# Kernel optimization log

Hardware: AMD Instinct MI355X
Metric: run time of the kernel (lower is better)

## Reference

```python
import jax, jax.numpy as jnp
import numpy as np

LN_EPS = 1e-5

def setup_inputs() -> dict:
    key = jax.random.key(0)
    ks = jax.random.split(key, 10)
    L, B, D, C, O = 512, 2, 256, 128, 64
    s_in = 1.0 / np.sqrt(D)
    s_ch = 1.0 / np.sqrt(C)
    return {
        "x": jax.random.normal(ks[0], (L, B, D), dtype=jnp.float32),
        "ln_gamma": jnp.ones((D,), dtype=jnp.float32),
        "ln_beta": jnp.zeros((D,), dtype=jnp.float32),
        "w1": jax.random.uniform(ks[1], (D, C), jnp.float32, -s_in, s_in),
        "b1": jax.random.uniform(ks[2], (C,), jnp.float32, -s_in, s_in),
        "w2": jax.random.uniform(ks[3], (D, C), jnp.float32, -s_in, s_in),
        "b2": jax.random.uniform(ks[4], (C,), jnp.float32, -s_in, s_in),
        "w3": jax.random.uniform(ks[5], (C, O), jnp.float32, -s_ch, s_ch),
        "b3": jax.random.uniform(ks[6], (O,), jnp.float32, -s_ch, s_ch),
        "w4": jax.random.uniform(ks[7], (C, O), jnp.float32, -s_ch, s_ch),
    }

def _layernorm(x, gamma, beta):
    mu = jnp.mean(x, axis=-1, keepdims=True)
    var = jnp.mean(jnp.square(x - mu), axis=-1, keepdims=True)
    return (x - mu) * jax.lax.rsqrt(var + LN_EPS) * gamma + beta

def reference(x, ln_gamma, ln_beta, w1, b1, w2, b2, w3, b3, w4):
    # x: (L, B, D) -> (B, L, D)
    xb = jnp.transpose(x, (1, 0, 2))
    xb = _layernorm(xb, ln_gamma, ln_beta)
    a = xb @ w1 + b1  # (B, L, C)
    b = xb @ w2 + b2  # (B, L, C)
    # (a_l * b_m) @ w3  -> contract channel dim directly into output channels
    mul_term = jnp.einsum('blc,bmc,co->blmo', a, b, w3) + b3
    # (a_l - b_m) @ w4  -> distribute linearity to avoid (B,L,L,C) materialization
    a4 = a @ w4  # (B, L, O)
    b4 = b @ w4  # (B, L, O)
    sub_term = a4[:, :, None, :] - b4[:, None, :, :]
    return mul_term + sub_term  # (B, L, L, O)
```

## Files before the change

### kernel.cpp

```cpp
#include <hip/hip_runtime.h>
#include <hip/hip_bf16.h>

#define LL 512
#define BB 2
#define DD 256
#define CC 128
#define OO 64

typedef __attribute__((ext_vector_type(8))) short bf16x8;
typedef __attribute__((ext_vector_type(4))) float f32x4;

__device__ __forceinline__ short f2bf(float v) {
    __hip_bfloat16 h = __float2bfloat16(v);
    return *reinterpret_cast<short*>(&h);
}
__device__ __forceinline__ float bf2f(short s) {
    __hip_bfloat16 h;
    *reinterpret_cast<short*>(&h) = s;
    return __bfloat162float(h);
}

__device__ __forceinline__ float wave_reduce_sum(float v) {
#pragma unroll
    for (int off = 32; off > 0; off >>= 1)
        v += __shfl_down(v, off, 64);
    return v;
}

__global__ __launch_bounds__(256) void prep_kernel(
    const float* __restrict__ x,
    const float* __restrict__ gamma,
    const float* __restrict__ beta,
    const float* __restrict__ w1, const float* __restrict__ b1,
    const float* __restrict__ w2, const float* __restrict__ b2,
    const float* __restrict__ w4, const float* __restrict__ b3,
    const float* __restrict__ w3,
    float* __restrict__ a_ws, short* __restrict__ bact,
    float* __restrict__ a4b3_ws, float* __restrict__ b4_ws,
    short* __restrict__ w3s)
{
    const int blk = blockIdx.x;
    const int t = threadIdx.x;

    if (blk >= BB * LL) {
        const int e  = (blk - BB * LL) * 256 + t;
        const int j  = e & 7;
        const int ln = (e >> 3) & 15;
        const int q  = (e >> 7) & 3;
        const int ks = (e >> 9) & 3;
        const int ot = e >> 11;
        const int c = ks * 32 + q * 8 + j;
        const int o = ot * 16 + ln;
        w3s[e] = f2bf(w3[c * OO + o]);
        return;
    }

    const int b = blk >> 9;
    const int l = blk & (LL - 1);

    __shared__ float ylds[DD];
    __shared__ float ab[2 * CC];
    __shared__ float red[8];

    float xv = x[(l * BB + b) * DD + t];
    float s = wave_reduce_sum(xv);
    if ((t & 63) == 0) red[t >> 6] = s;
    __syncthreads();
    float mu = (red[0] + red[1] + red[2] + red[3]) * (1.0f / DD);
    float xc = xv - mu;
    float s2 = wave_reduce_sum(xc * xc);
    if ((t & 63) == 0) red[4 + (t >> 6)] = s2;
    __syncthreads();
    float var = (red[4] + red[5] + red[6] + red[7]) * (1.0f / DD);
    float y = xc * rsqrtf(var + 1e-5f) * gamma[t] + beta[t];
    ylds[t] = y;
    __syncthreads();

    {
        const int c = t & (CC - 1);
        const float* w = (t < CC) ? w1 : w2;
        const float4* y4 = (const float4*)ylds;
        float acc0 = (t < CC) ? b1[c] : b2[c];
        float acc1 = 0.f, acc2 = 0.f, acc3 = 0.f;
#pragma unroll
        for (int i = 0; i < 64; i += 4) {
            float4 ya = y4[i], yb = y4[i + 1], yc = y4[i + 2], yd = y4[i + 3];
            const float* wp = w + i * 4 * CC + c;
            acc0 = fmaf(ya.x, wp[0 * CC], acc0);
            acc0 = fmaf(ya.y, wp[1 * CC], acc0);
            acc0 = fmaf(ya.z, wp[2 * CC], acc0);
            acc0 = fmaf(ya.w, wp[3 * CC], acc0);
            acc1 = fmaf(yb.x, wp[4 * CC], acc1);
            acc1 = fmaf(yb.y, wp[5 * CC], acc1);
            acc1 = fmaf(yb.z, wp[6 * CC], acc1);
            acc1 = fmaf(yb.w, wp[7 * CC], acc1);
            acc2 = fmaf(yc.x, wp[8 * CC], acc2);
            acc2 = fmaf(yc.y, wp[9 * CC], acc2);
            acc2 = fmaf(yc.z, wp[10 * CC], acc2);
            acc2 = fmaf(yc.w, wp[11 * CC], acc2);
            acc3 = fmaf(yd.x, wp[12 * CC], acc3);
            acc3 = fmaf(yd.y, wp[13 * CC], acc3);
            acc3 = fmaf(yd.z, wp[14 * CC], acc3);
            acc3 = fmaf(yd.w, wp[15 * CC], acc3);
        }
        float accv = (acc0 + acc1) + (acc2 + acc3);
        ab[t] = accv;
        if (t < CC) a_ws[(b * LL + l) * CC + c] = accv;
        else        bact[(b * LL + l) * CC + c] = f2bf(accv);
    }
    __syncthreads();

    if (t < 2 * OO) {
        const int o = t & (OO - 1);
        const float4* s4 = (const float4*)((t < OO) ? ab : (ab + CC));
        float acc0 = (t < OO) ? b3[o] : 0.0f;
        float acc1 = 0.f, acc2 = 0.f, acc3 = 0.f;
#pragma unroll
        for (int i = 0; i < 32; i += 4) {
            float4 sa = s4[i], sb = s4[i + 1], sc = s4[i + 2], sd = s4[i + 3];
            const float* wp = w4 + i * 4 * OO + o;
            acc0 = fmaf(sa.x, wp[0 * OO], acc0);
            acc0 = fmaf(sa.y, wp[1 * OO], acc0);
            acc0 = fmaf(sa.z, wp[2 * OO], acc0);
            acc0 = fmaf(sa.w, wp[3 * OO], acc0);
            acc1 = fmaf(sb.x, wp[4 * OO], acc1);
            acc1 = fmaf(sb.y, wp[5 * OO], acc1);
            acc1 = fmaf(sb.z, wp[6 * OO], acc1);
            acc1 = fmaf(sb.w, wp[7 * OO], acc1);
            acc2 = fmaf(sc.x, wp[8 * OO], acc2);
            acc2 = fmaf(sc.y, wp[9 * OO], acc2);
            acc2 = fmaf(sc.z, wp[10 * OO], acc2);
            acc2 = fmaf(sc.w, wp[11 * OO], acc2);
            acc3 = fmaf(sd.x, wp[12 * OO], acc3);
            acc3 = fmaf(sd.y, wp[13 * OO], acc3);
            acc3 = fmaf(sd.z, wp[14 * OO], acc3);
            acc3 = fmaf(sd.w, wp[15 * OO], acc3);
        }
        float accv = (acc0 + acc1) + (acc2 + acc3);
        ((t < OO) ? a4b3_ws : b4_ws)[(b * LL + l) * OO + o] = accv;
    }
}

__global__ __launch_bounds__(256, 3) void main_kernel(
    const float* __restrict__ a_ws, const short* __restrict__ bact,
    const float* __restrict__ a4b3_ws, const float* __restrict__ b4_ws,
    const short* __restrict__ w3s,
    float* __restrict__ out)
{
    const int bid = blockIdx.x;
    const int mh = bid & 1;
    const int l  = (bid >> 1) & (LL - 1);
    const int b  = bid >> 10;
    const int t  = threadIdx.x;
    const int wave = t >> 6;
    const int lane = t & 63;
    const int ln = lane & 15;
    const int q  = lane >> 4;
    const int mbase = mh * 256 + wave * 64;

    const float* arow = a_ws + (b * LL + l) * CC;
    const short* abase = bact + (size_t)(b * LL + mbase + ln) * CC + q * 8;

    f32x4 acc[4][4];
#pragma unroll
    for (int ot = 0; ot < 4; ++ot)
#pragma unroll
        for (int mt = 0; mt < 4; ++mt)
            acc[ot][mt] = (f32x4){0.f, 0.f, 0.f, 0.f};

#pragma unroll
    for (int ks = 0; ks < 4; ++ks) {
        const float* ap = arow + ks * 32 + q * 8;
        float av[8];
        *(float4*)&av[0] = *(const float4*)ap;
        *(float4*)&av[4] = *(const float4*)(ap + 4);

        bf16x8 wp[4];
#pragma unroll
        for (int ot = 0; ot < 4; ++ot) {
            bf16x8 wr = *(const bf16x8*)(w3s + (((ot * 4 + ks) * 4 + q) << 7) + ln * 8);
            bf16x8 r;
#pragma unroll
            for (int j = 0; j < 8; ++j)
                r[j] = f2bf(bf2f(wr[j]) * av[j]);
            wp[ot] = r;
        }

        bf16x8 bfr[4];
#pragma unroll
        for (int mt = 0; mt < 4; ++mt)
            bfr[mt] = *(const bf16x8*)(abase + mt * 16 * CC + ks * 32);

#pragma unroll
        for (int ot = 0; ot < 4; ++ot)
#pragma unroll
            for (int mt = 0; mt < 4; ++mt)
                acc[ot][mt] = __builtin_amdgcn_mfma_f32_16x16x32_bf16(
                    wp[ot], bfr[mt], acc[ot][mt], 0, 0, 0);
    }

    const float* a4p = a4b3_ws + (b * LL + l) * OO;
    float4 a4v[4];
#pragma unroll
    for (int ot = 0; ot < 4; ++ot)
        a4v[ot] = *(const float4*)(a4p + ot * 16 + q * 4);

#pragma unroll
    for (int mt = 0; mt < 4; ++mt) {
        const int m = mbase + mt * 16 + ln;
        const float* b4p = b4_ws + (size_t)(b * LL + m) * OO;
        float* op = out + ((size_t)(b * LL + l) * LL + m) * OO;
#pragma unroll
        for (int ot = 0; ot < 4; ++ot) {
            float4 bq = *(const float4*)(b4p + ot * 16 + q * 4);
            f32x4 a = acc[ot][mt];
            float4 r;
            r.x = a[0] + a4v[ot].x - bq.x;
            r.y = a[1] + a4v[ot].y - bq.y;
            r.z = a[2] + a4v[ot].z - bq.z;
            r.w = a[3] + a4v[ot].w - bq.w;
            *(float4*)(op + ot * 16 + q * 4) = r;
        }
    }
}

extern "C" void kernel_launch(void* const* d_in, const int* in_sizes, int n_in,
                              void* d_out, int out_size, void* d_ws, size_t ws_size,
                              hipStream_t stream) {
    const float* x     = (const float*)d_in[0];
    const float* gamma = (const float*)d_in[1];
    const float* beta  = (const float*)d_in[2];
    const float* w1    = (const float*)d_in[3];
    const float* b1    = (const float*)d_in[4];
    const float* w2    = (const float*)d_in[5];
    const float* b2    = (const float*)d_in[6];
    const float* w3    = (const float*)d_in[7];
    const float* b3    = (const float*)d_in[8];
    const float* w4    = (const float*)d_in[9];
    float* out = (float*)d_out;

    char* ws = (char*)d_ws;
    float* a_ws    = (float*)ws;
    short* bact    = (short*)(ws + 512 * 1024);
    float* a4b3_ws = (float*)(ws + 768 * 1024);
    float* b4_ws   = (float*)(ws + 1024 * 1024);
    short* w3s     = (short*)(ws + 1280 * 1024);

    prep_kernel<<<BB * LL + 32, 256, 0, stream>>>(x, gamma, beta, w1, b1, w2, b2,
                                                  w4, b3, w3,
                                                  a_ws, bact, a4b3_ws, b4_ws, w3s);
    main_kernel<<<BB * LL * 2, 256, 0, stream>>>(a_ws, bact, a4b3_ws, b4_ws,
                                                 w3s, out);
}
```

Baseline: 194.2 us.

## Precompute per-row scaled W3 fragments in a separate kernel before main GEMM

Adds a wall_kernel that precomputes, for every (b,l) row, W3 scaled elementwise by a[b,l,:] in bf16 and stores it in an extra 16 MB workspace buffer. The main kernel then loads these fragments directly instead of recomputing the bf16 scale-and-convert per MFMA operand. The goal is to cut VALU conversion work and register pressure in the hot loop, and the launch bound rises from 3 to 4 blocks per SIMD. In exchange it adds a kernel launch and about 16 MB of extra global write and read traffic.

```diff
diff --git a/kernel.cpp b/kernel.cpp
--- a/kernel.cpp
+++ b/kernel.cpp
@@ -141,10 +141,38 @@
     }
 }
 
-__global__ __launch_bounds__(256, 3) void main_kernel(
-    const float* __restrict__ a_ws, const short* __restrict__ bact,
+__global__ __launch_bounds__(256) void wall_kernel(
+    const float* __restrict__ a_ws, const short* __restrict__ w3s,
+    short* __restrict__ wall)
+{
+    const int blk = blockIdx.x;
+    const int t = threadIdx.x;
+    const int f0 = t * 4;
+    const int q  = (f0 >> 4) & 3;
+    const int ks = (f0 >> 6) & 3;
+    const int c  = ks * 32 + q * 8;
+
+    const float* ap = a_ws + blk * CC + c;
+    float av[8];
+    *(float4*)&av[0] = *(const float4*)ap;
+    *(float4*)&av[4] = *(const float4*)(ap + 4);
+
+    const short* src = w3s + f0 * 8;
+    short* dst = wall + (size_t)blk * (CC * OO) + f0 * 8;
+#pragma unroll
+    for (int i = 0; i < 4; ++i) {
+        bf16x8 wr = *(const bf16x8*)(src + i * 8);
+        bf16x8 r;
+#pragma unroll
+        for (int j = 0; j < 8; ++j)
+            r[j] = f2bf(bf2f(wr[j]) * av[j]);
+        *(bf16x8*)(dst + i * 8) = r;
+    }
+}
+
+__global__ __launch_bounds__(256, 4) void main_kernel(
+    const short* __restrict__ wall, const short* __restrict__ bact,
     const float* __restrict__ a4b3_ws, const float* __restrict__ b4_ws,
-    const short* __restrict__ w3s,
     float* __restrict__ out)
 {
     const int bid = blockIdx.x;
@@ -158,7 +186,7 @@
     const int q  = lane >> 4;
     const int mbase = mh * 256 + wave * 64;
 
-    const float* arow = a_ws + (b * LL + l) * CC;
+    const short* wbase = wall + (size_t)(b * LL + l) * (CC * OO) + (q * 16 + ln) * 8;
     const short* abase = bact + (size_t)(b * LL + mbase + ln) * CC + q * 8;
 
     f32x4 acc[4][4];
@@ -170,33 +198,19 @@
 
 #pragma unroll
     for (int ks = 0; ks < 4; ++ks) {
-        const float* ap = arow + ks * 32 + q * 8;
-        float av[8];
-        *(float4*)&av[0] = *(const float4*)ap;
-        *(float4*)&av[4] = *(const float4*)(ap + 4);
-
-        bf16x8 wp[4];
-#pragma unroll
-        for (int ot = 0; ot < 4; ++ot) {
-            bf16x8 wr = *(const bf16x8*)(w3s + (((ot * 4 + ks) * 4 + q) << 7) + ln * 8);
-            bf16x8 r;
-#pragma unroll
-            for (int j = 0; j < 8; ++j)
-                r[j] = f2bf(bf2f(wr[j]) * av[j]);
-            wp[ot] = r;
-        }
-
-        bf16x8 bfr[4];
+        bf16x8 wf[4], bfr[4];
+#pragma unroll
+        for (int ot = 0; ot < 4; ++ot)
+            wf[ot] = *(const bf16x8*)(wbase + (ot * 4 + ks) * 512);
 #pragma unroll
         for (int mt = 0; mt < 4; ++mt)
             bfr[mt] = *(const bf16x8*)(abase + mt * 16 * CC + ks * 32);
-
 #pragma unroll
         for (int ot = 0; ot < 4; ++ot)
 #pragma unroll
             for (int mt = 0; mt < 4; ++mt)
                 acc[ot][mt] = __builtin_amdgcn_mfma_f32_16x16x32_bf16(
-                    wp[ot], bfr[mt], acc[ot][mt], 0, 0, 0);
+                    wf[ot], bfr[mt], acc[ot][mt], 0, 0, 0);
     }
 
     const float* a4p = a4b3_ws + (b * LL + l) * OO;
@@ -245,10 +259,11 @@
     float* a4b3_ws = (float*)(ws + 768 * 1024);
     float* b4_ws   = (float*)(ws + 1024 * 1024);
     short* w3s     = (short*)(ws + 1280 * 1024);
+    short* wall    = (short*)(ws + 2048 * 1024);
 
     prep_kernel<<<BB * LL + 32, 256, 0, stream>>>(x, gamma, beta, w1, b1, w2, b2,
                                                   w4, b3, w3,
                                                   a_ws, bact, a4b3_ws, b4_ws, w3s);
-    main_kernel<<<BB * LL * 2, 256, 0, stream>>>(a_ws, bact, a4b3_ws, b4_ws,
-                                                 w3s, out);
-}
+    wall_kernel<<<BB * LL, 256, 0, stream>>>(a_ws, w3s, wall);
+    main_kernel<<<BB * LL * 2, 256, 0, stream>>>(wall, bact, a4b3_ws, b4_ws, out);
+}
```

Measured after the change: 210.7 us. 8.5% more time.
